# Optimization experiments

Measured on AMD Instinct MI355X. Metric: run time of the kernel, lower is better.

## Reference

```python
import jax, jax.numpy as jnp
import numpy as np

NAN_FILL = 9999999999.0


def setup_inputs() -> dict:
    key = jax.random.key(0)
    k_x, k_c = jax.random.split(key)
    b, c, s, k = 16, 512, 2048, 8192
    x = jax.random.normal(k_x, (b, c, s), dtype=jnp.float32)
    centroids = jax.random.normal(k_c, (c, k), dtype=jnp.float32)  # [c, k]
    return {"x": x, "centroids": centroids}


def reference(x, centroids):
    # x: [b, c, s] -> [b*s, c]
    b, c, s = x.shape
    xf = jnp.transpose(x, (0, 2, 1)).reshape(b * s, c)
    x_sq = jnp.sum(xf * xf, axis=1, keepdims=True)
    c_sq = jnp.sum(centroids * centroids, axis=0, keepdims=True)
    distances = x_sq - 2.0 * (xf @ centroids) + c_sq
    distances = jnp.where(jnp.isnan(distances), NAN_FILL, distances)
    distances = distances.reshape(b, s, centroids.shape[-1])
    labels = jnp.argmin(distances, axis=-1)  # [b, s] int
    return labels
```

## Files before the change

### kernel.cpp

```cpp
#include <hip/hip_runtime.h>
#include <hip/hip_fp16.h>

typedef _Float16 half8 __attribute__((ext_vector_type(8)));
typedef float floatx4 __attribute__((ext_vector_type(4)));

#define TAU 0.25f
#define CMAX 128

#define BARRIER_LG() asm volatile("s_waitcnt lgkmcnt(0)\n\ts_barrier" ::: "memory")

__device__ inline unsigned long long score_key(float sc, int k) {
  unsigned uu = __float_as_uint(sc);
  uu ^= (unsigned)(((int)uu >> 31)) | 0x80000000u;
  return ((unsigned long long)uu << 32) | (unsigned)k;
}


__global__ void tsplit_x(const float* __restrict__ x, _Float16* __restrict__ xh) {
  __shared__ float tile[32][65];
  const int s0 = blockIdx.x * 64;
  const int c0 = blockIdx.y * 32;
  const int b = blockIdx.z;
  const int tx = threadIdx.x, ty = threadIdx.y;
  const float* src = x + ((size_t)b * 512 + c0) * 2048 + s0;
#pragma unroll
  for (int i = ty; i < 32; i += 8) {
    tile[i][tx] = src[(size_t)i * 2048 + tx];
    tile[i][tx + 32] = src[(size_t)i * 2048 + tx + 32];
  }
  __syncthreads();
  const int t = ty * 32 + tx;
  const int g = t >> 6;
  const int j = t & 63;
  half8 pk;
#pragma unroll
  for (int i = 0; i < 8; ++i) pk[i] = (_Float16)tile[g * 8 + i][j];
  const int row = b * 2048 + s0 + j;
  ((half8*)xh)[(size_t)(c0 / 8 + g) * 32768 + row] = pk;
}

__global__ void tsplit_c(const float* __restrict__ c, _Float16* __restrict__ cth) {
  __shared__ float tile[32][65];
  const int n0 = blockIdx.x * 64;
  const int c0 = blockIdx.y * 32;
  const int tx = threadIdx.x, ty = threadIdx.y;
#pragma unroll
  for (int i = ty; i < 32; i += 8) {
    tile[i][tx] = c[(size_t)(c0 + i) * 8192 + n0 + tx];
    tile[i][tx + 32] = c[(size_t)(c0 + i) * 8192 + n0 + tx + 32];
  }
  __syncthreads();
  const int t = ty * 32 + tx;
  const int g = t >> 6;
  const int j = t & 63;
  half8 pk;
#pragma unroll
  for (int i = 0; i < 8; ++i) pk[i] = (_Float16)tile[g * 8 + i][j];
  ((half8*)cth)[(size_t)(c0 / 8 + g) * 8192 + n0 + j] = pk;
}

__global__ void csq_kernel(const float* __restrict__ c, float* __restrict__ csq,
                           unsigned int* __restrict__ cnts) {
  __shared__ float red[256];
  const int t = threadIdx.x;
  if (blockIdx.x == 0 && t < 2) cnts[t] = 0u;
  const int nl = t & 63;
  const int cs = t >> 6;
  const int n = blockIdx.x * 64 + nl;
  float acc = 0.f;
  for (int cc = cs; cc < 512; cc += 4) {
    float v = c[(size_t)cc * 8192 + n];
    acc = fmaf(v, v, acc);
  }
  red[t] = acc;
  __syncthreads();
  if (t < 64) csq[n] = red[t] + red[t + 64] + red[t + 128] + red[t + 192];
}

__launch_bounds__(256, 4)
__global__ void gemm_top2(const _Float16* __restrict__ xh, const _Float16* __restrict__ cth,
                          const float* __restrict__ csq, float* __restrict__ pv1,
                          int* __restrict__ pi1, float* __restrict__ pv2) {
  __shared__ __align__(16) unsigned char smem[32768];
  __shared__ float ep_v1[128][2], ep_v2[128][2];
  __shared__ int ep_i1[128][2];

  const int t = threadIdx.x;
  const int m0 = blockIdx.x * 128;
  const int n0 = blockIdx.y * 128;

  const int srow = t & 127;
  const int kqp = t >> 7;
  const half8* Ag = (const half8*)xh + (size_t)(m0 + srow);
  const half8* Bg = (const half8*)cth + (size_t)(n0 + srow);

  const int l = t & 63;
  const int w = t >> 6;
  const int wm = w >> 1, wn = w & 1;
  const int l15 = l & 15, lq = l >> 4;
  const int aBase = lq * 128 + wm * 64 + l15;
  const int bBase = 512 + lq * 128 + wn * 64 + l15;

  floatx4 acc[4][4] = {};
  const half8* S = (const half8*)smem;
  half8* SW = (half8*)smem;

  half8 pfA0, pfA1, pfB0, pfB1;
  pfA0 = Ag[(size_t)(kqp)*32768];
  pfA1 = Ag[(size_t)(kqp + 2) * 32768];
  pfB0 = Bg[(size_t)(kqp)*8192];
  pfB1 = Bg[(size_t)(kqp + 2) * 8192];
  SW[t] = pfA0; SW[256 + t] = pfA1;
  SW[512 + t] = pfB0; SW[768 + t] = pfB1;
  pfA0 = Ag[(size_t)(4 + kqp) * 32768];
  pfA1 = Ag[(size_t)(4 + kqp + 2) * 32768];
  pfB0 = Bg[(size_t)(4 + kqp) * 8192];
  pfB1 = Bg[(size_t)(4 + kqp + 2) * 8192];

  for (int kc = 0; kc < 16; ++kc) {
    BARRIER_LG();
    const int bo = (kc & 1) * 1024;
    half8 a[4], b[4];
#pragma unroll
    for (int f = 0; f < 4; ++f) {
      a[f] = S[bo + aBase + f * 16];
      b[f] = S[bo + bBase + f * 16];
    }
#pragma unroll
    for (int mf = 0; mf < 4; ++mf)
#pragma unroll
      for (int nf = 0; nf < 4; ++nf)
        acc[mf][nf] = __builtin_amdgcn_mfma_f32_16x16x32_f16(b[nf], a[mf], acc[mf][nf], 0, 0, 0);
    if (kc < 15) {
      const int wo = ((kc + 1) & 1) * 1024;
      SW[wo + t] = pfA0; SW[wo + 256 + t] = pfA1;
      SW[wo + 512 + t] = pfB0; SW[wo + 768 + t] = pfB1;
      if (kc < 14) {
        const int o = (kc + 2) * 4;
        pfA0 = Ag[(size_t)(o + kqp) * 32768];
        pfA1 = Ag[(size_t)(o + kqp + 2) * 32768];
        pfB0 = Bg[(size_t)(o + kqp) * 8192];
        pfB1 = Bg[(size_t)(o + kqp + 2) * 8192];
      }
    }
  }

  floatx4 cs4[4];
  const floatx4* csq4 = (const floatx4*)csq;
#pragma unroll
  for (int nf = 0; nf < 4; ++nf)
    cs4[nf] = csq4[(n0 >> 2) + wn * 16 + nf * 4 + lq];

  const int siBase = n0 + wn * 64 + lq * 4;

#pragma unroll
  for (int mf = 0; mf < 4; ++mf) {
    float v1 = INFINITY, v2 = INFINITY;
    int i1 = 0;
#pragma unroll
    for (int nf = 0; nf < 4; ++nf) {
#pragma unroll
      for (int reg = 0; reg < 4; ++reg) {
        float sv = fmaf(-2.f, acc[mf][nf][reg], cs4[nf][reg]);
        int si = siBase + nf * 16 + reg;
        if (sv < v1) { v2 = v1; v1 = sv; i1 = si; }
        else if (sv < v2) { v2 = sv; }
      }
    }
#pragma unroll
    for (int off = 16; off <= 32; off <<= 1) {
      float w1 = __shfl_xor(v1, off, 64);
      int j1 = __shfl_xor(i1, off, 64);
      float w2 = __shfl_xor(v2, off, 64);
      if (w1 < v1 || (w1 == v1 && j1 < i1)) {
        v2 = fminf(v1, w2);
        v1 = w1; i1 = j1;
      } else {
        v2 = fminf(v2, w1);
      }
    }
    if (lq == 0) {
      int rl = wm * 64 + mf * 16 + l15;
      ep_v1[rl][wn] = v1;
      ep_i1[rl][wn] = i1;
      ep_v2[rl][wn] = v2;
    }
  }
  __syncthreads();
  if (t < 128) {
    float v1 = ep_v1[t][0], v2 = ep_v2[t][0];
    int i1 = ep_i1[t][0];
    float w1 = ep_v1[t][1], w2 = ep_v2[t][1];
    int j1 = ep_i1[t][1];
    if (w1 < v1 || (w1 == v1 && j1 < i1)) {
      v2 = fminf(v1, w2);
      v1 = w1; i1 = j1;
    } else {
      v2 = fminf(v2, w1);
    }
    const size_t o = (size_t)blockIdx.y * 32768 + m0 + t;
    pv1[o] = v1;
    pi1[o] = i1;
    pv2[o] = v2;
  }
}

__global__ void final_top2(const float* __restrict__ pv1, const int* __restrict__ pi1,
                           const float* __restrict__ pv2, int* __restrict__ out,
                           float* __restrict__ rowbest, unsigned int* __restrict__ cnt,
                           int* __restrict__ list) {
  __shared__ float sv1[8][33], sv2[8][33];
  __shared__ int si1[8][33];
  const int t = threadIdx.x;
  const int r = t & 31, c = t >> 5;
  const int row = blockIdx.x * 32 + r;
  float v1 = INFINITY, v2 = INFINITY;
  int i1 = 0;
#pragma unroll
  for (int k = 0; k < 8; ++k) {
    const size_t o = (size_t)(c * 8 + k) * 32768 + row;
    float w1 = pv1[o], w2 = pv2[o];
    int j1 = pi1[o];
    if (w1 < v1 || (w1 == v1 && j1 < i1)) {
      v2 = fminf(v1, w2);
      v1 = w1; i1 = j1;
    } else {
      v2 = fminf(v2, w1);
    }
  }
  sv1[c][r] = v1;
  sv2[c][r] = v2;
  si1[c][r] = i1;
  __syncthreads();
  if (c == 0) {
#pragma unroll
    for (int k = 1; k < 8; ++k) {
      float w1 = sv1[k][r], w2 = sv2[k][r];
      int j1 = si1[k][r];
      if (w1 < v1 || (w1 == v1 && j1 < i1)) {
        v2 = fminf(v1, w2);
        v1 = w1; i1 = j1;
      } else {
        v2 = fminf(v2, w1);
      }
    }
    out[row] = i1;
    rowbest[row] = v1;
    if (v2 - v1 < TAU) {
      unsigned int pos = atomicAdd(cnt, 1u);
      list[pos] = row;
    }
  }
}

__global__ void cand_refine(const float* __restrict__ x, const float* __restrict__ cen,
                            const float* __restrict__ csq, const float* __restrict__ pv1,
                            const int* __restrict__ pi1, const float* __restrict__ pv2,
                            const float* __restrict__ rowbest,
                            const unsigned int* __restrict__ cnt, const int* __restrict__ list,
                            unsigned int* __restrict__ cnt2, int* __restrict__ list2,
                            unsigned long long* __restrict__ slots, int* __restrict__ out) {
  __shared__ float xs[512];
  __shared__ int cand[CMAX];
  __shared__ int ccnt_s, needfull_s;
  __shared__ unsigned long long wbest[4];
  const int t = threadIdx.x;
  const int lane = t & 63, wid = t >> 6;
  const int n = (int)*cnt;
  for (int u = blockIdx.x; u < n; u += gridDim.x) {
    __syncthreads();
    const int row = list[u];
    const int b = row >> 11, s = row & 2047;
    if (t == 0) { ccnt_s = 0; needfull_s = 0; }
    __syncthreads();
    xs[t] = x[((size_t)(b * 512 + t)) * 2048 + s];
    xs[t + 256] = x[((size_t)(b * 512 + t + 256)) * 2048 + s];
    const float thr = rowbest[row] + TAU;
    if (t < 64) {
      const size_t o = (size_t)t * 32768 + row;
      float w1 = pv1[o];
      if (w1 < thr) {
        int p = atomicAdd(&ccnt_s, 1);
        if (p < CMAX) cand[p] = pi1[o];
        if (pv2[o] < thr) needfull_s = 1;
      }
    }
    __syncthreads();
    int ccnt = ccnt_s < CMAX ? ccnt_s : CMAX;
    unsigned long long best = ~0ULL;
    for (int ci = wid; ci < ccnt; ci += 4) {
      const int k = cand[ci];
      float p0 = 0.f, p1 = 0.f;
#pragma unroll
      for (int j = 0; j < 4; ++j)
        p0 = fmaf(xs[lane + 64 * j], cen[(size_t)(lane + 64 * j) * 8192 + k], p0);
#pragma unroll
      for (int j = 4; j < 8; ++j)
        p1 = fmaf(xs[lane + 64 * j], cen[(size_t)(lane + 64 * j) * 8192 + k], p1);
      float d = p0 + p1;
#pragma unroll
      for (int off = 32; off >= 1; off >>= 1) d += __shfl_xor(d, off, 64);
      unsigned long long key = score_key(fmaf(-2.f, d, csq[k]), k);
      if (key < best) best = key;
    }
    if (lane == 0) wbest[wid] = best;
    __syncthreads();
    if (t == 0) {
      unsigned long long m = wbest[0];
#pragma unroll
      for (int w2 = 1; w2 < 4; ++w2)
        if (wbest[w2] < m) m = wbest[w2];
      out[row] = (int)(unsigned)(m & 0xFFFFFFFFULL);
      if (needfull_s) {
        slots[row] = ~0ULL;
        unsigned int pos = atomicAdd(cnt2, 1u);
        list2[pos] = row;
      }
    }
  }
}

__global__ void fullscan(const float* __restrict__ x, const float* __restrict__ cen,
                         const float* __restrict__ csq, const unsigned int* __restrict__ cnt2,
                         const int* __restrict__ list2, unsigned long long* __restrict__ slots) {
  __shared__ float xs[512];
  __shared__ unsigned long long red[256];
  const int t = threadIdx.x;
  const int n2 = (int)*cnt2;
  const int units = n2 * 16;
  for (int u = blockIdx.x; u < units; u += gridDim.x) {
    __syncthreads();
    const int row = list2[u >> 4];
    const int sl = u & 15;
    const int b = row >> 11, s = row & 2047;
    xs[t] = x[((size_t)(b * 512 + t)) * 2048 + s];
    xs[t + 256] = x[((size_t)(b * 512 + t + 256)) * 2048 + s];
    __syncthreads();
    const int k0 = sl * 512 + t;
    float tot0 = 0.f, tot1 = 0.f;
#pragma unroll
    for (int ch = 0; ch < 4; ++ch) {
      float a0 = 0.f, a1 = 0.f;
      for (int c = ch * 128; c < ch * 128 + 128; ++c) {
        float xv = xs[c];
        a0 = fmaf(xv, cen[(size_t)c * 8192 + k0], a0);
        a1 = fmaf(xv, cen[(size_t)c * 8192 + k0 + 256], a1);
      }
      tot0 += a0;
      tot1 += a1;
    }
    unsigned long long k1 = score_key(fmaf(-2.f, tot0, csq[k0]), k0);
    unsigned long long k2 = score_key(fmaf(-2.f, tot1, csq[k0 + 256]), k0 + 256);
    red[t] = k1 < k2 ? k1 : k2;
    __syncthreads();
    for (int off = 128; off >= 1; off >>= 1) {
      if (t < off && red[t + off] < red[t]) red[t] = red[t + off];
      __syncthreads();
    }
    if (t == 0) atomicMin(&slots[row], red[0]);
  }
}

__global__ void fixup2(const unsigned int* __restrict__ cnt2, const int* __restrict__ list2,
                       const unsigned long long* __restrict__ slots, int* __restrict__ out) {
  const int n2 = (int)*cnt2;
  for (int i = blockIdx.x * blockDim.x + threadIdx.x; i < n2; i += blockDim.x * gridDim.x) {
    const int row = list2[i];
    out[row] = (int)(unsigned)(slots[row] & 0xFFFFFFFFULL);
  }
}

__global__ void fallback_kernel(const float* __restrict__ x, const float* __restrict__ cen,
                                int* __restrict__ out) {
  __shared__ float xrow[512];
  __shared__ float rv[256];
  __shared__ int ri[256];
  const int row = blockIdx.x;
  const int b = row >> 11, s = row & 2047;
  const int t = threadIdx.x;
  for (int c = t; c < 512; c += 256) xrow[c] = x[((size_t)b * 512 + c) * 2048 + s];
  __syncthreads();
  float bv = INFINITY;
  int bi = 0;
  for (int k = t; k < 8192; k += 256) {
    float d = 0.f;
    for (int c = 0; c < 512; ++c) {
      float diff = xrow[c] - cen[(size_t)c * 8192 + k];
      d = fmaf(diff, diff, d);
    }
    if (d < bv) { bv = d; bi = k; }
  }
  rv[t] = bv;
  ri[t] = bi;
  __syncthreads();
  for (int off = 128; off > 0; off >>= 1) {
    if (t < off) {
      if (rv[t + off] < rv[t] || (rv[t + off] == rv[t] && ri[t + off] < ri[t])) {
        rv[t] = rv[t + off];
        ri[t] = ri[t + off];
      }
    }
    __syncthreads();
  }
  if (t == 0) out[row] = ri[0];
}

extern "C" void kernel_launch(void* const* d_in, const int* in_sizes, int n_in,
                              void* d_out, int out_size, void* d_ws, size_t ws_size,
                              hipStream_t stream) {
  const float* x = (const float*)d_in[0];
  const float* cen = (const float*)d_in[1];
  int* out = (int*)d_out;

  const size_t XSZ = (size_t)32768 * 512;
  const size_t CSZ = (size_t)8192 * 512;
  const size_t OFF_CTH = XSZ * 2;
  const size_t OFF_CSQ = OFF_CTH + CSZ * 2;
  const size_t OFF_PV1 = OFF_CSQ + 8192 * 4;
  const size_t OFF_PI1 = OFF_PV1 + (size_t)64 * 32768 * 4;
  const size_t OFF_PV2 = OFF_PI1 + (size_t)64 * 32768 * 4;
  const size_t OFF_RB = OFF_PV2 + (size_t)64 * 32768 * 4;
  const size_t OFF_SLOT = OFF_RB + (size_t)32768 * 4;
  const size_t OFF_LIST = OFF_SLOT + (size_t)32768 * 8;
  const size_t OFF_LIST2 = OFF_LIST + (size_t)32768 * 4;
  const size_t OFF_CNT = OFF_LIST2 + (size_t)32768 * 4;
  const size_t NEED = OFF_CNT + 16;

  if (ws_size < NEED) {
    fallback_kernel<<<32768, 256, 0, stream>>>(x, cen, out);
    return;
  }

  char* ws = (char*)d_ws;
  _Float16* xh = (_Float16*)ws;
  _Float16* cth = (_Float16*)(ws + OFF_CTH);
  float* csq = (float*)(ws + OFF_CSQ);
  float* pv1 = (float*)(ws + OFF_PV1);
  int* pi1 = (int*)(ws + OFF_PI1);
  float* pv2 = (float*)(ws + OFF_PV2);
  float* rowbest = (float*)(ws + OFF_RB);
  unsigned long long* slots = (unsigned long long*)(ws + OFF_SLOT);
  int* list = (int*)(ws + OFF_LIST);
  int* list2 = (int*)(ws + OFF_LIST2);
  unsigned int* cnts = (unsigned int*)(ws + OFF_CNT);

  tsplit_x<<<dim3(32, 16, 16), dim3(32, 8), 0, stream>>>(x, xh);
  tsplit_c<<<dim3(128, 16), dim3(32, 8), 0, stream>>>(cen, cth);
  csq_kernel<<<128, 256, 0, stream>>>(cen, csq, cnts);
  gemm_top2<<<dim3(256, 64), 256, 0, stream>>>(xh, cth, csq, pv1, pi1, pv2);
  final_top2<<<1024, 256, 0, stream>>>(pv1, pi1, pv2, out, rowbest, cnts, list);
  cand_refine<<<512, 256, 0, stream>>>(x, cen, csq, pv1, pi1, pv2, rowbest,
                                       cnts, list, cnts + 1, list2, slots, out);
  fullscan<<<256, 256, 0, stream>>>(x, cen, csq, cnts + 1, list2, slots);
  fixup2<<<4, 256, 0, stream>>>(cnts + 1, list2, slots, out);
}
```

Baseline: 485.7 us.

## Write fp32 row-major transposes of x and centroids for coalesced refine loads

The transpose kernels now also emit fp32 row-major copies of x ([b*s, c]) and centroids ([k, c]) when the workspace is large enough. cand_refine and fullscan read x rows contiguously, and cand_refine reads centroid columns contiguously, instead of doing strided gathers with a 2048 or 8192 stride. The cost is about 80 MB of extra writes in the transpose kernels, which are paid on every call, to make the refinement loads for the candidate rows cheaper.

```diff
diff --git a/kernel.cpp b/kernel.cpp
--- a/kernel.cpp
+++ b/kernel.cpp
@@ -16,7 +16,8 @@
 }
 
 
-__global__ void tsplit_x(const float* __restrict__ x, _Float16* __restrict__ xh) {
+__global__ void tsplit_x(const float* __restrict__ x, _Float16* __restrict__ xh,
+                         float* __restrict__ xt) {
   __shared__ float tile[32][65];
   const int s0 = blockIdx.x * 64;
   const int c0 = blockIdx.y * 32;
@@ -30,16 +31,31 @@
   }
   __syncthreads();
   const int t = ty * 32 + tx;
-  const int g = t >> 6;
-  const int j = t & 63;
-  half8 pk;
-#pragma unroll
-  for (int i = 0; i < 8; ++i) pk[i] = (_Float16)tile[g * 8 + i][j];
-  const int row = b * 2048 + s0 + j;
-  ((half8*)xh)[(size_t)(c0 / 8 + g) * 32768 + row] = pk;
-}
-
-__global__ void tsplit_c(const float* __restrict__ c, _Float16* __restrict__ cth) {
+  {
+    const int g = t >> 6;
+    const int j = t & 63;
+    half8 pk;
+#pragma unroll
+    for (int i = 0; i < 8; ++i) pk[i] = (_Float16)tile[g * 8 + i][j];
+    const int row = b * 2048 + s0 + j;
+    ((half8*)xh)[(size_t)(c0 / 8 + g) * 32768 + row] = pk;
+  }
+  if (xt) {
+    const int jq = t >> 2, q = t & 3;
+    const int row = b * 2048 + s0 + jq;
+    floatx4 w0, w1;
+#pragma unroll
+    for (int i = 0; i < 4; ++i) w0[i] = tile[q * 8 + i][jq];
+#pragma unroll
+    for (int i = 0; i < 4; ++i) w1[i] = tile[q * 8 + 4 + i][jq];
+    floatx4* dst = (floatx4*)(xt + (size_t)row * 512 + c0 + q * 8);
+    dst[0] = w0;
+    dst[1] = w1;
+  }
+}
+
+__global__ void tsplit_c(const float* __restrict__ c, _Float16* __restrict__ cth,
+                         float* __restrict__ ct) {
   __shared__ float tile[32][65];
   const int n0 = blockIdx.x * 64;
   const int c0 = blockIdx.y * 32;
@@ -51,12 +67,25 @@
   }
   __syncthreads();
   const int t = ty * 32 + tx;
-  const int g = t >> 6;
-  const int j = t & 63;
-  half8 pk;
-#pragma unroll
-  for (int i = 0; i < 8; ++i) pk[i] = (_Float16)tile[g * 8 + i][j];
-  ((half8*)cth)[(size_t)(c0 / 8 + g) * 8192 + n0 + j] = pk;
+  {
+    const int g = t >> 6;
+    const int j = t & 63;
+    half8 pk;
+#pragma unroll
+    for (int i = 0; i < 8; ++i) pk[i] = (_Float16)tile[g * 8 + i][j];
+    ((half8*)cth)[(size_t)(c0 / 8 + g) * 8192 + n0 + j] = pk;
+  }
+  if (ct) {
+    const int jq = t >> 2, q = t & 3;
+    floatx4 w0, w1;
+#pragma unroll
+    for (int i = 0; i < 4; ++i) w0[i] = tile[q * 8 + i][jq];
+#pragma unroll
+    for (int i = 0; i < 4; ++i) w1[i] = tile[q * 8 + 4 + i][jq];
+    floatx4* dst = (floatx4*)(ct + (size_t)(n0 + jq) * 512 + c0 + q * 8);
+    dst[0] = w0;
+    dst[1] = w1;
+  }
 }
 
 __global__ void csq_kernel(const float* __restrict__ c, float* __restrict__ csq,
@@ -254,6 +283,7 @@
 }
 
 __global__ void cand_refine(const float* __restrict__ x, const float* __restrict__ cen,
+                            const float* __restrict__ xt, const float* __restrict__ ct,
                             const float* __restrict__ csq, const float* __restrict__ pv1,
                             const int* __restrict__ pi1, const float* __restrict__ pv2,
                             const float* __restrict__ rowbest,
@@ -273,8 +303,13 @@
     const int b = row >> 11, s = row & 2047;
     if (t == 0) { ccnt_s = 0; needfull_s = 0; }
     __syncthreads();
-    xs[t] = x[((size_t)(b * 512 + t)) * 2048 + s];
-    xs[t + 256] = x[((size_t)(b * 512 + t + 256)) * 2048 + s];
+    if (xt) {
+      xs[t] = xt[(size_t)row * 512 + t];
+      xs[t + 256] = xt[(size_t)row * 512 + t + 256];
+    } else {
+      xs[t] = x[((size_t)(b * 512 + t)) * 2048 + s];
+      xs[t + 256] = x[((size_t)(b * 512 + t + 256)) * 2048 + s];
+    }
     const float thr = rowbest[row] + TAU;
     if (t < 64) {
       const size_t o = (size_t)t * 32768 + row;
@@ -288,20 +323,39 @@
     __syncthreads();
     int ccnt = ccnt_s < CMAX ? ccnt_s : CMAX;
     unsigned long long best = ~0ULL;
-    for (int ci = wid; ci < ccnt; ci += 4) {
-      const int k = cand[ci];
-      float p0 = 0.f, p1 = 0.f;
-#pragma unroll
-      for (int j = 0; j < 4; ++j)
-        p0 = fmaf(xs[lane + 64 * j], cen[(size_t)(lane + 64 * j) * 8192 + k], p0);
-#pragma unroll
-      for (int j = 4; j < 8; ++j)
-        p1 = fmaf(xs[lane + 64 * j], cen[(size_t)(lane + 64 * j) * 8192 + k], p1);
-      float d = p0 + p1;
-#pragma unroll
-      for (int off = 32; off >= 1; off >>= 1) d += __shfl_xor(d, off, 64);
-      unsigned long long key = score_key(fmaf(-2.f, d, csq[k]), k);
-      if (key < best) best = key;
+    if (ct) {
+      for (int ci = wid; ci < ccnt; ci += 4) {
+        const int k = cand[ci];
+        const float* ck = ct + (size_t)k * 512;
+        float p0 = 0.f, p1 = 0.f;
+#pragma unroll
+        for (int j = 0; j < 4; ++j)
+          p0 = fmaf(xs[lane + 64 * j], ck[lane + 64 * j], p0);
+#pragma unroll
+        for (int j = 4; j < 8; ++j)
+          p1 = fmaf(xs[lane + 64 * j], ck[lane + 64 * j], p1);
+        float d = p0 + p1;
+#pragma unroll
+        for (int off = 32; off >= 1; off >>= 1) d += __shfl_xor(d, off, 64);
+        unsigned long long key = score_key(fmaf(-2.f, d, csq[k]), k);
+        if (key < best) best = key;
+      }
+    } else {
+      for (int ci = wid; ci < ccnt; ci += 4) {
+        const int k = cand[ci];
+        float p0 = 0.f, p1 = 0.f;
+#pragma unroll
+        for (int j = 0; j < 4; ++j)
+          p0 = fmaf(xs[lane + 64 * j], cen[(size_t)(lane + 64 * j) * 8192 + k], p0);
+#pragma unroll
+        for (int j = 4; j < 8; ++j)
+          p1 = fmaf(xs[lane + 64 * j], cen[(size_t)(lane + 64 * j) * 8192 + k], p1);
+        float d = p0 + p1;
+#pragma unroll
+        for (int off = 32; off >= 1; off >>= 1) d += __shfl_xor(d, off, 64);
+        unsigned long long key = score_key(fmaf(-2.f, d, csq[k]), k);
+        if (key < best) best = key;
+      }
     }
     if (lane == 0) wbest[wid] = best;
     __syncthreads();
@@ -321,6 +375,7 @@
 }
 
 __global__ void fullscan(const float* __restrict__ x, const float* __restrict__ cen,
+                         const float* __restrict__ xt,
                          const float* __restrict__ csq, const unsigned int* __restrict__ cnt2,
                          const int* __restrict__ list2, unsigned long long* __restrict__ slots) {
   __shared__ float xs[512];
@@ -333,8 +388,13 @@
     const int row = list2[u >> 4];
     const int sl = u & 15;
     const int b = row >> 11, s = row & 2047;
-    xs[t] = x[((size_t)(b * 512 + t)) * 2048 + s];
-    xs[t + 256] = x[((size_t)(b * 512 + t + 256)) * 2048 + s];
+    if (xt) {
+      xs[t] = xt[(size_t)row * 512 + t];
+      xs[t + 256] = xt[(size_t)row * 512 + t + 256];
+    } else {
+      xs[t] = x[((size_t)(b * 512 + t)) * 2048 + s];
+      xs[t + 256] = x[((size_t)(b * 512 + t + 256)) * 2048 + s];
+    }
     __syncthreads();
     const int k0 = sl * 512 + t;
     float tot0 = 0.f, tot1 = 0.f;
@@ -425,6 +485,9 @@
   const size_t OFF_LIST2 = OFF_LIST + (size_t)32768 * 4;
   const size_t OFF_CNT = OFF_LIST2 + (size_t)32768 * 4;
   const size_t NEED = OFF_CNT + 16;
+  const size_t OFF_XT = (NEED + 255) & ~(size_t)255;
+  const size_t OFF_CT = OFF_XT + (size_t)32768 * 512 * 4;
+  const size_t NEED_FULL = OFF_CT + (size_t)8192 * 512 * 4;
 
   if (ws_size < NEED) {
     fallback_kernel<<<32768, 256, 0, stream>>>(x, cen, out);
@@ -443,14 +506,17 @@
   int* list = (int*)(ws + OFF_LIST);
   int* list2 = (int*)(ws + OFF_LIST2);
   unsigned int* cnts = (unsigned int*)(ws + OFF_CNT);
-
-  tsplit_x<<<dim3(32, 16, 16), dim3(32, 8), 0, stream>>>(x, xh);
-  tsplit_c<<<dim3(128, 16), dim3(32, 8), 0, stream>>>(cen, cth);
+  const bool full = ws_size >= NEED_FULL;
+  float* xt = full ? (float*)(ws + OFF_XT) : nullptr;
+  float* ct = full ? (float*)(ws + OFF_CT) : nullptr;
+
+  tsplit_x<<<dim3(32, 16, 16), dim3(32, 8), 0, stream>>>(x, xh, xt);
+  tsplit_c<<<dim3(128, 16), dim3(32, 8), 0, stream>>>(cen, cth, ct);
   csq_kernel<<<128, 256, 0, stream>>>(cen, csq, cnts);
   gemm_top2<<<dim3(256, 64), 256, 0, stream>>>(xh, cth, csq, pv1, pi1, pv2);
   final_top2<<<1024, 256, 0, stream>>>(pv1, pi1, pv2, out, rowbest, cnts, list);
-  cand_refine<<<512, 256, 0, stream>>>(x, cen, csq, pv1, pi1, pv2, rowbest,
+  cand_refine<<<512, 256, 0, stream>>>(x, cen, xt, ct, csq, pv1, pi1, pv2, rowbest,
                                        cnts, list, cnts + 1, list2, slots, out);
-  fullscan<<<256, 256, 0, stream>>>(x, cen, csq, cnts + 1, list2, slots);
+  fullscan<<<256, 256, 0, stream>>>(x, cen, xt, csq, cnts + 1, list2, slots);
   fixup2<<<4, 256, 0, stream>>>(cnts + 1, list2, slots, out);
 }
```

Result: slower. 510.9 us (+5.2%).
